# Kernel tuning notes

Hardware: AMD Instinct MI355X
Metric: run time of the kernel (lower is better)

The kernel has to match this reference:

```python
import jax, jax.numpy as jnp
from jax import lax
import numpy as np

T = 100  # number of binarization thresholds, as in nn.Module (linspace(0,1,100))
THRESHOLDS = jnp.linspace(0.0, 1.0, T)


def _count_components(binimg):
    """4-connected component count per image via iterative min-label propagation.
    binimg: [N,H,W] float in {0,1}. Returns [N] int32 component counts.
    Equivalent math to the source's recursive DFS flood fill, vectorized."""
    N, H, W = binimg.shape
    fg = binimg > 0
    BIG = H * W  # sentinel label for background
    idx = jnp.arange(H * W, dtype=jnp.int32).reshape(H, W)
    lab0 = jnp.where(fg, idx[None], jnp.int32(BIG))

    def prop(lab):
        p = jnp.pad(lab, ((0, 0), (1, 1), (1, 1)), constant_values=BIG)
        nmin = jnp.minimum(jnp.minimum(p[:, :-2, 1:-1], p[:, 2:, 1:-1]),
                           jnp.minimum(p[:, 1:-1, :-2], p[:, 1:-1, 2:]))
        return jnp.where(fg, jnp.minimum(lab, nmin), jnp.int32(BIG))

    def cond(c):
        return ~c[1]

    def body(c):
        lab = c[0]
        new = prop(prop(prop(lab)))  # 3 propagation steps per convergence check
        return (new, jnp.all(new == lab))

    lab, _ = lax.while_loop(cond, body, (lab0, jnp.array(False)))
    # each component keeps exactly one pixel whose label equals its own index
    return jnp.sum(fg & (lab == idx[None]), axis=(1, 2)).astype(jnp.int32)


def _betti(prob):
    """prob: [R,H,W] -> [T,R,2] (b0, b1) per threshold per region.
    b1 = b0 - euler, euler = #pixels - #4-neighbor edges (as in source)."""
    R, H, W = prob.shape
    binz = (prob[None] > THRESHOLDS[:, None, None, None]).astype(jnp.float32)  # [T,R,H,W]
    flat = binz.reshape(T * R, H, W)
    b0 = lax.stop_gradient(_count_components(flat)).astype(jnp.float32).reshape(T, R)
    pix = flat.sum((1, 2))
    edges = (flat[:, :-1] * flat[:, 1:]).sum((1, 2)) + (flat[:, :, :-1] * flat[:, :, 1:]).sum((1, 2))
    euler = (pix - edges).reshape(T, R)
    b1 = b0 - euler
    return jnp.stack([b0, b1], axis=-1)  # [T,R,2]


def setup_inputs() -> dict:
    key = jax.random.key(0)
    k1, k2 = jax.random.split(key)
    three_class_prob = jax.random.uniform(k1, (4, 3, 128, 128), dtype=jnp.float32)
    selected_regions = jnp.arange(4, dtype=jnp.int64)
    gt_barcodes = jax.random.uniform(k2, (4, 6, T - 1, 2), dtype=jnp.float32)
    return {"three_class_prob": three_class_prob,
            "selected_regions": selected_regions,
            "gt_barcodes": gt_barcodes}


def reference(three_class_prob, selected_regions, gt_barcodes):
    sel = three_class_prob[selected_regions]  # [R,3,H,W]
    inside = _betti(sel[:, 0])     # channel 0
    boundary = _betti(sel[:, 1])   # channel 1
    union = inside                 # source uses channel 0:1 again -> same values
    codes = jnp.concatenate([inside, boundary, union], axis=-1)  # [T,R,6]
    # barcode extraction: birth at increases of the betti curve, death at decreases
    d = codes[1:] - codes[:-1]                 # [T-1,R,6]
    th = THRESHOLDS[:-1, None, None]
    birth = jnp.where(d > 0, th, 0.0)
    death = jnp.where(d < 0, th, 0.0)
    barcodes = jnp.stack([birth, death], axis=-1).transpose(1, 2, 0, 3)  # [R,6,T-1,2]
    # fixed-shape matching: pair barcodes sorted by birth time (Hungarian surrogate)
    ord_b = jnp.argsort(barcodes[..., 0], axis=-1)
    ord_g = jnp.argsort(gt_barcodes[..., 0], axis=-1)
    bs = jnp.take_along_axis(barcodes, ord_b[..., None], axis=-2)
    gs = jnp.take_along_axis(gt_barcodes, ord_g[..., None], axis=-2)
    matched_diff = jnp.sum(jnp.abs(bs - gs), axis=-1)                  # [R,6,T-1]
    unmatched_len = jnp.sum(barcodes[..., 1] - barcodes[..., 0], axis=-1)  # [R,6]
    return jnp.mean(matched_diff) + jnp.mean(unmatched_len)
```

## Files before the change

### kernel.cpp

```cpp
#include <hip/hip_runtime.h>

typedef unsigned long long u64;

__device__ __forceinline__ int find_root(int* L, int a){
    int p = L[a];
    while(p != a){
        int gp = L[p];
        if(gp != p) L[a] = gp;
        a = p; p = gp;
    }
    return a;
}

__device__ __forceinline__ int unite(int* L, int a, int b){
    while(true){
        a = find_root(L, a);
        b = find_root(L, b);
        if(a == b) return 0;
        int hi = (a > b) ? a : b;
        int lo = (a > b) ? b : a;
        int old = atomicCAS(&L[hi], hi, lo);
        if(old == hi) return 1;
        a = old; b = lo;
    }
}

__global__ __launch_bounds__(256) void ccl_kernel(const float* __restrict__ prob,
                                                  const int*   __restrict__ sel,
                                                  float*       __restrict__ betti,
                                                  float*       __restrict__ out){
    __shared__ u64 M[256];
    __shared__ u64 S[256];
    __shared__ int Pr[257];
    __shared__ int L[6400];
    __shared__ int red[12];
    const int tid = threadIdx.x, bid = blockIdx.x;
    if(bid == 0 && tid == 0) atomicExch(out, 0.0f);
    const int ch = bid / 400, t = (bid % 400) >> 2, r = bid & 3;
    const float th = (float)t / 99.0f;
    const float* img = prob + (size_t)(sel[r] * 3 + ch) * 16384;

    const int w = tid;
    {
        const float4* imgv = (const float4*)img;
        u64 mw = 0ULL;
        #pragma unroll
        for(int k = 0; k < 16; k++){
            const float4 v = imgv[w * 16 + k];
            const unsigned nib = (unsigned)(v.x > th)
                               | ((unsigned)(v.y > th) << 1)
                               | ((unsigned)(v.z > th) << 2)
                               | ((unsigned)(v.w > th) << 3);
            mw |= (u64)nib << (4 * k);
        }
        M[w] = mw;
    }
    __syncthreads();

    const int lane = tid & 63, wave = tid >> 6;
    const int row = w >> 1, half = w & 1;
    const u64 m = M[w];
    const u64 lcar = half ? (M[w - 1] >> 63) : 0ULL;
    const u64 s = m & ~((m << 1) | lcar);
    S[w] = s;
    int pix   = __popcll(m);
    int edges = __popcll(m & ((m << 1) | lcar));
    const u64 va = (row > 0) ? M[w - 2] : 0ULL;
    edges += __popcll(m & va);
    const int runs = __popcll(s);
    u64 csm = 0ULL;
    if(row > 0){
        const u64 c = m & va;
        const u64 ccar = half ? ((M[w - 1] & M[w - 3]) >> 63) : 0ULL;
        csm = c & ~((c << 1) | ccar);
    }

    int incl = runs;
    for(int off = 1; off < 64; off <<= 1){
        int n = __shfl_up(incl, off, 64);
        if(lane >= off) incl += n;
    }
    if(lane == 63) red[wave] = incl;
    __syncthreads();
    int woff = 0;
    for(int k = 0; k < wave; k++) woff += red[k];
    const int excl = woff + incl - runs;
    Pr[w] = excl;
    if(w == 255) Pr[256] = excl + runs;
    const u64 sa = (row > 0) ? S[w - 2] : 0ULL;
    __syncthreads();
    const int R = Pr[256];
    const int Pa = (row > 0) ? Pr[w - 2] : 0;

    {
        int4* L4 = (int4*)L;
        const int n4 = (R + 3) >> 2;
        for(int i = tid; i < n4; i += 256){ int b = i * 4; L4[i] = make_int4(b, b+1, b+2, b+3); }
    }
    __syncthreads();

    int merges = 0;
    {
        u64 cs = csm;
        while(cs){
            const int x = __ffsll(cs) - 1;
            cs &= cs - 1;
            const u64 lm = (2ULL << x) - 1;
            const int nb = excl + __popcll(s  & lm) - 1;
            const int na = Pa   + __popcll(sa & lm) - 1;
            merges += unite(L, na, nb);
        }
    }

    int v0 = pix, v1 = edges, v2 = merges;
    for(int off = 32; off; off >>= 1){
        v0 += __shfl_down(v0, off, 64);
        v1 += __shfl_down(v1, off, 64);
        v2 += __shfl_down(v2, off, 64);
    }
    __syncthreads();
    if(lane == 0){ red[wave*3] = v0; red[wave*3+1] = v1; red[wave*3+2] = v2; }
    __syncthreads();
    if(tid == 0){
        int P = 0, E = 0, MG = 0;
        for(int k = 0; k < 4; k++){ P += red[k*3]; E += red[k*3+1]; MG += red[k*3+2]; }
        const float b0f = (float)(R - MG);
        const float b1f = b0f - ((float)P - (float)E);
        const size_t o = (((size_t)ch * 100 + t) * 4 + r) * 2;
        betti[o] = b0f; betti[o + 1] = b1f;
    }
}

__global__ __launch_bounds__(128) void rows_kernel(const float* __restrict__ betti,
                                                   const float* __restrict__ gt,
                                                   float*       __restrict__ out){
    __shared__ float codes[100];
    __shared__ float birth[99], bs0[99], bs1[99], gs0[99], gs1[99];
    __shared__ float gsh[198];
    __shared__ float red[4];
    const int row = blockIdx.x;
    const int r = row / 6, j = row % 6;
    const int chmap[6] = {0, 0, 1, 1, 0, 0};
    const int ch = chmap[j], comp = j & 1;
    const int tid = threadIdx.x;

    if(tid < 100) codes[tid] = betti[(((size_t)ch * 100 + tid) * 4 + r) * 2 + comp];
    const float* g = gt + (size_t)row * 99 * 2;
    for(int i = tid; i < 198; i += 128) gsh[i] = g[i];
    __syncthreads();

    float b = 0.f, d = 0.f;
    if(tid < 99){
        const float dv = codes[tid + 1] - codes[tid];
        const float thv = (float)tid / 99.0f;
        b = (dv > 0.f) ? thv : 0.f;
        d = (dv < 0.f) ? thv : 0.f;
        birth[tid] = b;
    }
    __syncthreads();

    if(tid < 99){
        int zb = 0, tz = 0;
        for(int k = 0; k < 99; k++){
            const int z = (birth[k] == 0.f) ? 1 : 0;
            tz += z;
            if(k < tid) zb += z;
        }
        const int pos = (b == 0.f) ? zb : (tz + tid - zb);
        bs0[pos] = b; bs1[pos] = d;

        const float gb = gsh[tid * 2];
        int rank = 0;
        for(int k = 0; k < 99; k++){
            const float o = gsh[k * 2];
            rank += (o < gb || (o == gb && k < tid)) ? 1 : 0;
        }
        gs0[rank] = gb; gs1[rank] = gsh[tid * 2 + 1];
    }
    __syncthreads();

    float mm = 0.f, u = 0.f;
    if(tid < 99){
        mm = fabsf(bs0[tid] - gs0[tid]) + fabsf(bs1[tid] - gs1[tid]);
        u = d - b;
    }
    for(int off = 32; off; off >>= 1){
        mm += __shfl_down(mm, off, 64);
        u  += __shfl_down(u,  off, 64);
    }
    if((tid & 63) == 0){ red[(tid >> 6)*2] = mm; red[(tid >> 6)*2 + 1] = u; }
    __syncthreads();
    if(tid == 0)
        atomicAdd(out, (red[0] + red[2]) / 2376.0f + (red[1] + red[3]) / 24.0f);
}

extern "C" void kernel_launch(void* const* d_in, const int* in_sizes, int n_in,
                              void* d_out, int out_size, void* d_ws, size_t ws_size,
                              hipStream_t stream){
    const float* prob = (const float*)d_in[0];
    const int*   sel  = (const int*)d_in[1];
    const float* gt   = (const float*)d_in[2];
    float* betti = (float*)d_ws;

    ccl_kernel <<<800, 256, 0, stream>>>(prob, sel, betti, (float*)d_out);
    rows_kernel<<<24, 128, 0, stream>>>(betti, gt, (float*)d_out);
}
```

Measured before the change: 93.06 us.

## Fuse CCL and barcode kernels into one cooperative launch with grid sync

```diff
diff --git a/kernel.cpp b/kernel.cpp
--- a/kernel.cpp
+++ b/kernel.cpp
@@ -1,5 +1,7 @@
 #include <hip/hip_runtime.h>
-
+#include <hip/hip_cooperative_groups.h>
+
+namespace cg = cooperative_groups;
 typedef unsigned long long u64;
 
 __device__ __forceinline__ int find_root(int* L, int a){
@@ -25,16 +27,12 @@
     }
 }
 
-__global__ __launch_bounds__(256) void ccl_kernel(const float* __restrict__ prob,
-                                                  const int*   __restrict__ sel,
-                                                  float*       __restrict__ betti,
-                                                  float*       __restrict__ out){
-    __shared__ u64 M[256];
-    __shared__ u64 S[256];
-    __shared__ int Pr[257];
-    __shared__ int L[6400];
-    __shared__ int red[12];
-    const int tid = threadIdx.x, bid = blockIdx.x;
+__device__ __forceinline__ void ccl_body(const float* __restrict__ prob,
+                                         const int*   __restrict__ sel,
+                                         float*       __restrict__ betti,
+                                         float*       __restrict__ out,
+                                         u64* M, u64* S, int* Pr, int* L, int* red,
+                                         int tid, int bid){
     if(bid == 0 && tid == 0) atomicExch(out, 0.0f);
     const int ch = bid / 400, t = (bid % 400) >> 2, r = bid & 3;
     const float th = (float)t / 99.0f;
@@ -127,26 +125,32 @@
         const float b0f = (float)(R - MG);
         const float b1f = b0f - ((float)P - (float)E);
         const size_t o = (((size_t)ch * 100 + t) * 4 + r) * 2;
-        betti[o] = b0f; betti[o + 1] = b1f;
-    }
-}
-
-__global__ __launch_bounds__(128) void rows_kernel(const float* __restrict__ betti,
-                                                   const float* __restrict__ gt,
-                                                   float*       __restrict__ out){
-    __shared__ float codes[100];
-    __shared__ float birth[99], bs0[99], bs1[99], gs0[99], gs1[99];
-    __shared__ float gsh[198];
-    __shared__ float red[4];
-    const int row = blockIdx.x;
+        __hip_atomic_store(&betti[o],     b0f, __ATOMIC_RELAXED, __HIP_MEMORY_SCOPE_AGENT);
+        __hip_atomic_store(&betti[o + 1], b1f, __ATOMIC_RELAXED, __HIP_MEMORY_SCOPE_AGENT);
+    }
+}
+
+__device__ __forceinline__ void rows_body(const float* __restrict__ betti,
+                                          const float* __restrict__ gt,
+                                          float*       __restrict__ out,
+                                          int row, int tid, float* fsh){
+    float* codes = fsh;
+    float* birth = fsh + 100;
+    float* bs0   = fsh + 199;
+    float* bs1   = fsh + 298;
+    float* gs0   = fsh + 397;
+    float* gs1   = fsh + 496;
+    float* gsh   = fsh + 595;
+    float* redf  = fsh + 793;
     const int r = row / 6, j = row % 6;
     const int chmap[6] = {0, 0, 1, 1, 0, 0};
     const int ch = chmap[j], comp = j & 1;
-    const int tid = threadIdx.x;
-
-    if(tid < 100) codes[tid] = betti[(((size_t)ch * 100 + tid) * 4 + r) * 2 + comp];
-    const float* g = gt + (size_t)row * 99 * 2;
-    for(int i = tid; i < 198; i += 128) gsh[i] = g[i];
+
+    if(tid < 100)
+        codes[tid] = __hip_atomic_load(&betti[(((size_t)ch * 100 + tid) * 4 + r) * 2 + comp],
+                                       __ATOMIC_RELAXED, __HIP_MEMORY_SCOPE_AGENT);
+    const float* g = gt + (size_t)row * 198;
+    for(int i = tid; i < 198; i += 256) gsh[i] = g[i];
     __syncthreads();
 
     float b = 0.f, d = 0.f;
@@ -188,10 +192,49 @@
         mm += __shfl_down(mm, off, 64);
         u  += __shfl_down(u,  off, 64);
     }
-    if((tid & 63) == 0){ red[(tid >> 6)*2] = mm; red[(tid >> 6)*2 + 1] = u; }
+    if((tid & 63) == 0){ redf[(tid >> 6) * 2] = mm; redf[(tid >> 6) * 2 + 1] = u; }
     __syncthreads();
     if(tid == 0)
-        atomicAdd(out, (red[0] + red[2]) / 2376.0f + (red[1] + red[3]) / 24.0f);
+        atomicAdd(out, (redf[0] + redf[2] + redf[4] + redf[6]) / 2376.0f
+                     + (redf[1] + redf[3] + redf[5] + redf[7]) / 24.0f);
+}
+
+__global__ __launch_bounds__(256, 4) void fused_kernel(const float* __restrict__ prob,
+                                                       const int*   __restrict__ sel,
+                                                       const float* __restrict__ gt,
+                                                       float*       __restrict__ betti,
+                                                       float*       __restrict__ out){
+    __shared__ u64 M[256];
+    __shared__ u64 S[256];
+    __shared__ int Pr[257];
+    __shared__ int L[6400];
+    __shared__ int red[12];
+    const int tid = threadIdx.x, bid = blockIdx.x;
+
+    ccl_body(prob, sel, betti, out, M, S, Pr, L, red, tid, bid);
+
+    cg::this_grid().sync();
+
+    if(bid < 24) rows_body(betti, gt, out, bid, tid, (float*)L);
+}
+
+__global__ __launch_bounds__(256) void ccl_kernel(const float* __restrict__ prob,
+                                                  const int*   __restrict__ sel,
+                                                  float*       __restrict__ betti,
+                                                  float*       __restrict__ out){
+    __shared__ u64 M[256];
+    __shared__ u64 S[256];
+    __shared__ int Pr[257];
+    __shared__ int L[6400];
+    __shared__ int red[12];
+    ccl_body(prob, sel, betti, out, M, S, Pr, L, red, threadIdx.x, blockIdx.x);
+}
+
+__global__ __launch_bounds__(256) void rows_kernel(const float* __restrict__ betti,
+                                                   const float* __restrict__ gt,
+                                                   float*       __restrict__ out){
+    __shared__ float fsh[801];
+    rows_body(betti, gt, out, blockIdx.x, threadIdx.x, fsh);
 }
 
 extern "C" void kernel_launch(void* const* d_in, const int* in_sizes, int n_in,
@@ -201,7 +244,14 @@
     const int*   sel  = (const int*)d_in[1];
     const float* gt   = (const float*)d_in[2];
     float* betti = (float*)d_ws;
-
-    ccl_kernel <<<800, 256, 0, stream>>>(prob, sel, betti, (float*)d_out);
-    rows_kernel<<<24, 128, 0, stream>>>(betti, gt, (float*)d_out);
-}
+    float* outp  = (float*)d_out;
+
+    void* args[5] = { (void*)&prob, (void*)&sel, (void*)&gt, (void*)&betti, (void*)&outp };
+    hipError_t err = hipLaunchCooperativeKernel((const void*)fused_kernel,
+                                                dim3(800), dim3(256),
+                                                (void**)args, 0u, stream);
+    if(err != hipSuccess){
+        ccl_kernel <<<800, 256, 0, stream>>>(prob, sel, betti, outp);
+        rows_kernel<<<24, 256, 0, stream>>>(betti, gt, outp);
+    }
+}
```

Measured after the change: 173.8 us. 86.7% more time.
